# Kernel tuning notes

Measured on AMD Instinct MI355X. Metric: run time of the kernel, lower is better.

The kernel has to match this reference:

```python
import jax, jax.numpy as jnp
import numpy as np

H, DK = 8, 64  # n_head, d_k = n_feat // n_head
SCALE = 1.0 / np.sqrt(DK)


def setup_inputs() -> dict:
    key0 = jax.random.key(0)
    ks = jax.random.split(key0, 13)
    B, N, T1, T2, F = 16, 4, 256, 1024, 512
    query = jax.random.normal(ks[0], (B, T1, F), jnp.float32)
    key = jax.random.normal(ks[1], (B, N, T2, F), jnp.float32)
    value = jax.random.normal(ks[2], (B, N, T2, F), jnp.float32)
    mask_audio = jax.random.randint(ks[3], (B, N, 1, T2), 0, 2).astype(jnp.int32)
    # guarantee each candidate row has at least one valid key frame
    mask_audio = mask_audio.at[..., 0].set(1)
    mask_spk = jax.random.randint(ks[4], (B, N), 0, 2).astype(jnp.int32)
    # guarantee at least one valid candidate per batch item (avoids all -inf softmax)
    mask_spk = mask_spk.at[:, 0].set(1)
    s = 1.0 / np.sqrt(F)
    Wq = jax.random.normal(ks[5], (F, F), jnp.float32) * s
    bq = jax.random.normal(ks[6], (F,), jnp.float32) * 0.01
    Wk = jax.random.normal(ks[7], (F, F), jnp.float32) * s
    bk = jax.random.normal(ks[8], (F,), jnp.float32) * 0.01
    Wv = jax.random.normal(ks[9], (F, F), jnp.float32) * s
    bv = jax.random.normal(ks[10], (F,), jnp.float32) * 0.01
    Wo = jax.random.normal(ks[11], (F, F), jnp.float32) * s
    bo = jax.random.normal(ks[12], (F,), jnp.float32) * 0.01
    return dict(query=query, key=key, value=value, mask_audio=mask_audio,
                mask_spk=mask_spk, Wq=Wq, bq=bq, Wk=Wk, bk=bk, Wv=Wv, bv=bv,
                Wo=Wo, bo=bo)


def reference(query, key, value, mask_audio, mask_spk, Wq, bq, Wk, bk, Wv, bv, Wo, bo):
    B, T1, F = query.shape
    N, T2 = key.shape[1], key.shape[2]
    # projections (torch Linear: x @ W.T + b)
    q = (query @ Wq.T + bq).reshape(B, T1, H, DK)                 # (B,T1,H,DK)
    k = (key @ Wk.T + bk).reshape(B, N, T2, H, DK)                # (B,N,T2,H,DK)
    v = (value @ Wv.T + bv).reshape(B, N, T2, H, DK)
    # stage 1: intra-candidate temporal attention
    scores = jnp.einsum('bthd,bnshd->bnhts', q, k) * SCALE        # (B,N,H,T1,T2)
    ma = (mask_audio != 0)[:, :, None, :, :]                      # (B,N,1,1,T2)
    scores = jnp.where(ma, scores, -jnp.inf)
    attn1 = jnp.where(ma, jax.nn.softmax(scores, axis=-1), 0.0)
    phone = jnp.einsum('bnhts,bnshd->bnhtd', attn1, v)            # (B,N,H,T1,DK)
    # stage 2: inter-candidate attention
    ss = jnp.einsum('bthd,bnhtd->bthn', q, phone) * SCALE         # (B,T1,H,N)
    ms = (mask_spk != 0)[:, None, None, :]                        # (B,1,1,N)
    ss = jnp.where(ms, ss, -jnp.inf)
    attn2 = jnp.where(ms, jax.nn.softmax(ss, axis=-1), 0.0)
    x = jnp.einsum('bthn,bnhtd->bthd', attn2, phone).reshape(B, T1, H * DK)
    return x @ Wo.T + bo
```

## Files before the change

### kernel.cpp

```cpp
#include <hip/hip_runtime.h>
#include <hip/hip_bf16.h>
#include <math.h>

typedef __attribute__((ext_vector_type(4))) float  f32x4;
typedef __attribute__((ext_vector_type(4))) int    i32x4;
typedef __attribute__((ext_vector_type(8))) __bf16 bf16x8;
typedef __attribute__((ext_vector_type(8))) unsigned short u16x8;
typedef __attribute__((ext_vector_type(4))) unsigned short u16x4;

#define DEV static __device__ __forceinline__

#if __has_builtin(__builtin_amdgcn_permlane32_swap) && __has_builtin(__builtin_amdgcn_permlane16_swap)
#define HAVE_PERMLANE 1
#else
#define HAVE_PERMLANE 0
#endif

namespace {

constexpr int kB = 16, kT1 = 256, kF = 512, kN = 4, kT2 = 1024, kH = 8;
constexpr float kSCALE = 0.125f;
constexpr float kLOG2E = 1.4426950408889634f;

DEV unsigned short f2bf(float f) {
  union { __bf16 h; unsigned short u; } c; c.h = (__bf16)f; return c.u;
}
DEV float bf2f(unsigned short h) {
  union { unsigned u; float f; } c; c.u = ((unsigned)h) << 16;
  return c.f;
}

DEV void async_copy16(const void* g, void* l) {
  __builtin_amdgcn_global_load_lds(
      (const __attribute__((address_space(1))) unsigned int*)g,
      (__attribute__((address_space(3))) unsigned int*)l, 16, 0, 0);
}

DEV bf16x8 cvt8(f32x4 lo, f32x4 hi) {
  bf16x8 r;
  r[0] = (__bf16)lo[0]; r[1] = (__bf16)lo[1]; r[2] = (__bf16)lo[2]; r[3] = (__bf16)lo[3];
  r[4] = (__bf16)hi[0]; r[5] = (__bf16)hi[1]; r[6] = (__bf16)hi[2]; r[7] = (__bf16)hi[3];
  return r;
}

__global__ __launch_bounds__(256) void convert_w(
    const float* __restrict__ w0, const float* __restrict__ w1,
    const float* __restrict__ w2, const float* __restrict__ w3,
    unsigned short* __restrict__ o0, unsigned short* __restrict__ o1,
    unsigned short* __restrict__ o2, unsigned short* __restrict__ o3) {
  const int r = blockIdx.x >> 8;
  const int l = ((blockIdx.x & 255) * 256 + threadIdx.x) * 4;
  const float* src = r == 0 ? w0 : r == 1 ? w1 : r == 2 ? w2 : w3;
  unsigned short* dst = r == 0 ? o0 : r == 1 ? o1 : r == 2 ? o2 : o3;
  const float4 v = *(const float4*)(src + l);
  u16x4 q; q[0] = f2bf(v.x); q[1] = f2bf(v.y); q[2] = f2bf(v.z); q[3] = f2bf(v.w);
  *(u16x4*)(dst + l) = q;
}

template<int MODE>
__global__ __launch_bounds__(512, 2) void gemm256(
    const float* __restrict__ A, const unsigned short* __restrict__ Wb,
    const float* __restrict__ bias, unsigned short* __restrict__ outv) {
  __shared__ __align__(16) unsigned short As[2][256 * 64];
  __shared__ __align__(16) unsigned short Ws[2][256 * 64];
  const int t = threadIdx.x, lane = t & 63, wave = t >> 6;
  const int rb = blockIdx.x >> 1, cb = blockIdx.x & 1;
  const int wr = wave >> 2, wc = wave & 3;
  const int lq = lane & 15, lg = lane >> 4;
  const int arg = t >> 4, as16 = t & 15;

  f32x4 acc[8][4];
#pragma unroll
  for (int i = 0; i < 8; ++i)
#pragma unroll
    for (int j = 0; j < 4; ++j) acc[i][j] = f32x4{0.f, 0.f, 0.f, 0.f};

  f32x4 areg[8];
  bf16x8 af[4][2], bf[4][2];

#define A_ISSUE(kt)                                                             \
  do {                                                                          \
    _Pragma("unroll")                                                           \
    for (int j_ = 0; j_ < 8; ++j_)                                              \
      areg[j_] = *(const f32x4*)(A + (size_t)(rb * 256 + j_ * 32 + arg) * kF +  \
                                 (kt) * 64 + as16 * 4);                         \
  } while (0)

#define A_WRITE(dst)                                                            \
  do {                                                                          \
    _Pragma("unroll")                                                           \
    for (int j_ = 0; j_ < 8; ++j_) {                                            \
      const int row_ = j_ * 32 + arg;                                           \
      const int off_ = row_ * 64 + (((as16 >> 1) ^ (row_ & 7)) << 3) + (as16 & 1) * 4; \
      u16x4 pk_;                                                                \
      pk_[0] = f2bf(areg[j_][0]); pk_[1] = f2bf(areg[j_][1]);                   \
      pk_[2] = f2bf(areg[j_][2]); pk_[3] = f2bf(areg[j_][3]);                   \
      *(u16x4*)&(dst)[off_] = pk_;                                              \
    }                                                                           \
  } while (0)

#define W_ISSUE(kt, dst)                                                        \
  do {                                                                          \
    _Pragma("unroll")                                                           \
    for (int j_ = 0; j_ < 4; ++j_) {                                            \
      const int sidx_ = t + j_ * 512;                                           \
      const int row_ = sidx_ >> 3, s_ = sidx_ & 7;                              \
      async_copy16(Wb + (size_t)(cb * 256 + row_) * kF + (kt) * 64 +            \
                       ((s_ ^ (row_ & 7)) << 3),                                \
                   (dst) + (size_t)(j_ * 512 + wave * 64) * 8);                 \
    }                                                                           \
  } while (0)

#define RD_BF(pw)                                                               \
  do {                                                                          \
    _Pragma("unroll")                                                           \
    for (int n_ = 0; n_ < 4; ++n_) {                                            \
      const int br_ = wc * 64 + n_ * 16 + lq, x7_ = br_ & 7;                    \
      bf[n_][0] = *(const bf16x8*)&(pw)[br_ * 64 + ((lg ^ x7_) << 3)];          \
      bf[n_][1] = *(const bf16x8*)&(pw)[br_ * 64 + (((4 + lg) ^ x7_) << 3)];    \
    }                                                                           \
  } while (0)

#define RD_AF(pa, mb)                                                           \
  do {                                                                          \
    _Pragma("unroll")                                                           \
    for (int m_ = 0; m_ < 4; ++m_) {                                            \
      const int ar_ = wr * 128 + ((mb) + m_) * 16 + lq, x7_ = ar_ & 7;          \
      af[m_][0] = *(const bf16x8*)&(pa)[ar_ * 64 + ((lg ^ x7_) << 3)];          \
      af[m_][1] = *(const bf16x8*)&(pa)[ar_ * 64 + (((4 + lg) ^ x7_) << 3)];    \
    }                                                                           \
  } while (0)

#define MM(mb)                                                                  \
  do {                                                                          \
    _Pragma("unroll")                                                           \
    for (int kk_ = 0; kk_ < 2; ++kk_)                                           \
      _Pragma("unroll")                                                         \
      for (int m_ = 0; m_ < 4; ++m_)                                            \
        _Pragma("unroll")                                                       \
        for (int n_ = 0; n_ < 4; ++n_)                                          \
          acc[(mb) + m_][n_] = __builtin_amdgcn_mfma_f32_16x16x32_bf16(         \
              af[m_][kk_], bf[n_][kk_], acc[(mb) + m_][n_], 0, 0, 0);           \
  } while (0)

#define VMW(n) asm volatile("s_waitcnt vmcnt(" #n ")" ::: "memory")
#define LKW  asm volatile("s_waitcnt lgkmcnt(0)" ::: "memory")
#define SB   __builtin_amdgcn_sched_barrier(0)
#define BAR  do { __builtin_amdgcn_s_barrier(); __builtin_amdgcn_sched_barrier(0); } while (0)

  A_ISSUE(0); W_ISSUE(0, Ws[0]);
  VMW(4); SB;
  A_WRITE(As[0]);
  LKW;

  unsigned short *pa = As[0], *qa = As[1], *pw = Ws[0], *qw = Ws[1];
#pragma unroll 1
  for (int kt = 0; kt < 8; ++kt) {
    if (kt < 7) {
      A_ISSUE(kt + 1);
      W_ISSUE(kt + 1, qw);
      VMW(12); SB;
    } else {
      VMW(0); SB;
    }
    BAR;
    RD_BF(pw); RD_AF(pa, 0);
    LKW; SB;
    __builtin_amdgcn_s_setprio(1); MM(0); __builtin_amdgcn_s_setprio(0); SB;
    RD_AF(pa, 4);
    LKW; SB;
    __builtin_amdgcn_s_setprio(1); MM(4); __builtin_amdgcn_s_setprio(0); SB;
    if (kt < 7) {
      VMW(4); SB;
      A_WRITE(qa);
    }
    LKW; BAR;
    { unsigned short* x = pa; pa = qa; qa = x; }
    { unsigned short* x = pw; pw = qw; qw = x; }
  }

#undef A_ISSUE
#undef A_WRITE
#undef W_ISSUE
#undef RD_BF
#undef RD_AF
#undef MM
#undef VMW
#undef LKW
#undef SB
#undef BAR

  float bs4[4];
#pragma unroll
  for (int n = 0; n < 4; ++n) bs4[n] = bias[cb * 256 + wc * 64 + n * 16 + lq];

#pragma unroll
  for (int m = 0; m < 8; ++m) {
    const int row0 = rb * 256 + wr * 128 + m * 16 + lg * 4;
    const int bn = row0 >> 10, t2 = row0 & 1023;
#pragma unroll
    for (int n = 0; n < 4; ++n) {
      const int col = cb * 256 + wc * 64 + n * 16 + lq;
      const int h = col >> 6, d = col & 63;
      if (MODE == 3) {
        u16x4 pv;
#pragma unroll
        for (int j = 0; j < 4; ++j) pv[j] = f2bf(acc[m][n][j] + bs4[n]);
        *(u16x4*)&outv[(((size_t)(bn * kH + h)) * 64 + d) * kT2 + t2] = pv;
      } else {
#pragma unroll
        for (int j = 0; j < 4; ++j)
          outv[(((size_t)(bn * kH + h)) * kT2 + t2 + j) * 64 + d] =
              f2bf(acc[m][n][j] + bs4[n]);
      }
    }
  }
}

template<int MODE>
__global__ __launch_bounds__(256, 2) void gemm_mixed(
    const float* __restrict__ A, const unsigned short* __restrict__ Wb,
    const float* __restrict__ bias, void* __restrict__ outv, int nrb) {
  __shared__ __align__(16) unsigned short As[2][128 * 64];
  __shared__ __align__(16) unsigned short Bs[3][128 * 64];
  const int t = threadIdx.x, lane = t & 63, wave = t >> 6;
  const int w = blockIdx.x;
  const int xcd = w & 7, s = w >> 3;
  const int rb = xcd * (nrb >> 3) + (s >> 2);
  const int cb = s & 3;
  const int wr = wave >> 1, wc = wave & 1;
  const int lq = lane & 15, lg = lane >> 4;

  const int arow = t >> 1, ah = (t & 1) * 4;
  const float* aptr = A + (size_t)(rb * 128 + arow) * kF + ah * 8;

  f32x4 acc[4][4];
#pragma unroll
  for (int i = 0; i < 4; ++i)
#pragma unroll
    for (int j = 0; j < 4; ++j) acc[i][j] = f32x4{0.f, 0.f, 0.f, 0.f};

  f32x4 arA[8], arB[8];
  bf16x8 af[4][2], bfr[4][2];

#define A_LOAD(kb, ar)                                                          \
  do {                                                                          \
    const f32x4* p_ = (const f32x4*)(aptr + (kb) * 64);                         \
    ar[0]=p_[0]; ar[1]=p_[1]; ar[2]=p_[2]; ar[3]=p_[3];                         \
    ar[4]=p_[4]; ar[5]=p_[5]; ar[6]=p_[6]; ar[7]=p_[7];                         \
  } while (0)

#define A_CVT(ar, dst)                                                          \
  do {                                                                          \
    _Pragma("unroll")                                                           \
    for (int j_ = 0; j_ < 4; ++j_)                                              \
      *(bf16x8*)&(dst)[arow * 64 + (((ah + j_) ^ (arow & 7)) << 3)] =           \
          cvt8(ar[2*j_], ar[2*j_+1]);                                           \
  } while (0)

#define W_STAGE2(kb, dst)                                                       \
  do {                                                                          \
    _Pragma("unroll")                                                           \
    for (int i_ = 0; i_ < 4; ++i_) {                                            \
      const int sidx_ = t + i_ * 256;                                           \
      const int row_ = sidx_ >> 3;                                              \
      const int gseg_ = (sidx_ & 7) ^ (row_ & 7);                               \
      async_copy16(Wb + (size_t)(cb * 128 + row_) * kF + (kb) * 64 + gseg_ * 8, \
                   (dst) + (size_t)(i_ * 256 + wave * 64) * 8);                 \
    }                                                                           \
  } while (0)

#define FRAG(Ap, Wp)                                                            \
  do {                                                                          \
    _Pragma("unroll")                                                           \
    for (int m_ = 0; m_ < 4; ++m_) {                                            \
      const int ar_ = wr * 64 + m_ * 16 + lq, x7_ = ar_ & 7;                    \
      af[m_][0] = *(const bf16x8*)&(Ap)[ar_ * 64 + ((lg       ^ x7_) << 3)];    \
      af[m_][1] = *(const bf16x8*)&(Ap)[ar_ * 64 + (((lg + 4) ^ x7_) << 3)];    \
    }                                                                           \
    _Pragma("unroll")                                                           \
    for (int n_ = 0; n_ < 4; ++n_) {                                            \
      const int br_ = wc * 64 + n_ * 16 + lq, x7_ = br_ & 7;                    \
      bfr[n_][0] = *(const bf16x8*)&(Wp)[br_ * 64 + ((lg       ^ x7_) << 3)];   \
      bfr[n_][1] = *(const bf16x8*)&(Wp)[br_ * 64 + (((lg + 4) ^ x7_) << 3)];   \
    }                                                                           \
  } while (0)

#define MFMA8                                                                   \
  do {                                                                          \
    _Pragma("unroll")                                                           \
    for (int kk_ = 0; kk_ < 2; ++kk_)                                           \
      _Pragma("unroll")                                                         \
      for (int m_ = 0; m_ < 4; ++m_)                                            \
        _Pragma("unroll")                                                       \
        for (int n_ = 0; n_ < 4; ++n_)                                          \
          acc[m_][n_] = __builtin_amdgcn_mfma_f32_16x16x32_bf16(                \
              af[m_][kk_], bfr[n_][kk_], acc[m_][n_], 0, 0, 0);                 \
  } while (0)

#define VMW(n) asm volatile("s_waitcnt vmcnt(" #n ")" ::: "memory")
#define LKW    asm volatile("s_waitcnt lgkmcnt(0)" ::: "memory")
#define BAR    do { __builtin_amdgcn_s_barrier(); __builtin_amdgcn_sched_barrier(0); } while (0)

  A_LOAD(0, arA); A_LOAD(1, arB);
  W_STAGE2(0, Bs[0]); W_STAGE2(1, Bs[1]);
  VMW(16);
  A_CVT(arA, As[0]);
  LKW; BAR;
  A_LOAD(2, arA); W_STAGE2(2, Bs[2]);
  FRAG(As[0], Bs[0]); MFMA8;
  VMW(12); A_CVT(arB, As[1]); LKW; BAR;
  A_LOAD(3, arB); W_STAGE2(3, Bs[0]);
  FRAG(As[1], Bs[1]); MFMA8;
  VMW(12); A_CVT(arA, As[0]); LKW; BAR;
  A_LOAD(4, arA); W_STAGE2(4, Bs[1]);
  FRAG(As[0], Bs[2]); MFMA8;
  VMW(12); A_CVT(arB, As[1]); LKW; BAR;
  A_LOAD(5, arB); W_STAGE2(5, Bs[2]);
  FRAG(As[1], Bs[0]); MFMA8;
  VMW(12); A_CVT(arA, As[0]); LKW; BAR;
  A_LOAD(6, arA); W_STAGE2(6, Bs[0]);
  FRAG(As[0], Bs[1]); MFMA8;
  VMW(12); A_CVT(arB, As[1]); LKW; BAR;
  A_LOAD(7, arB); W_STAGE2(7, Bs[1]);
  FRAG(As[1], Bs[2]); MFMA8;
  VMW(12); A_CVT(arA, As[0]); LKW; BAR;
  FRAG(As[0], Bs[0]); MFMA8;
  VMW(0); A_CVT(arB, As[1]); LKW; BAR;
  FRAG(As[1], Bs[1]); MFMA8;

#undef A_LOAD
#undef A_CVT
#undef W_STAGE2
#undef FRAG
#undef MFMA8
#undef VMW
#undef LKW
#undef BAR

  float bs[4];
#pragma unroll
  for (int n2 = 0; n2 < 4; ++n2) bs[n2] = bias[cb*128 + wc*64 + n2*16 + lq];

#pragma unroll
  for (int m = 0; m < 4; ++m) {
#pragma unroll
    for (int n2 = 0; n2 < 4; ++n2) {
      const int col = cb*128 + wc*64 + n2*16 + lq;
      const int row0 = rb*128 + wr*64 + m*16 + lg*4;
#pragma unroll
      for (int j = 0; j < 4; ++j) {
        const int row = row0 + j;
        const float v = acc[m][n2][j] + bs[n2];
        if (MODE == 2) {
          ((float*)outv)[(size_t)row * kF + col] = v;
        } else {
          const int h = col >> 6, d = col & 63;
          const int b = row >> 8, t1i = row & 255;
          ((unsigned short*)outv)[(((size_t)(b * kH + h)) * kT1 + t1i) * 64 + d] = f2bf(v);
        }
      }
    }
  }
}

__global__ __launch_bounds__(512, 4) void attn_kernel(
    const unsigned short* __restrict__ qh, const unsigned short* __restrict__ kh,
    const unsigned short* __restrict__ vt, const int* __restrict__ mask_audio,
    unsigned short* __restrict__ phone) {
  __shared__ __align__(16) unsigned short Ks[3][64 * 64];
  __shared__ __align__(16) unsigned short Vs[3][64 * 64];
  __shared__ float Mbias[1024];
  const int t = threadIdx.x;
  const int lane = t & 63, wave = t >> 6;
  const int lq = lane & 15, lg = lane >> 4;
  const int bid = blockIdx.x;
  const int h = bid & 7, n = (bid >> 3) & 3, b = bid >> 5;
  const size_t qbase  = ((size_t)(b * kH + h)) * kT1 * 64;
  const size_t kvbase = ((size_t)((b * kN + n) * kH + h)) * kT2 * 64;
  const int* mbase = mask_audio + (size_t)(b * kN + n) * kT2;

  const int srow = (wave << 3) + (lane >> 3);
  const int sgx = ((lane & 7) ^ (srow & 7)) << 3;

#define STAGE_KV(c, kd, vd)                                                       \
  do {                                                                            \
    async_copy16(kh + kvbase + ((size_t)(((c) << 6) + srow) << 6) + sgx,          \
                 (kd) + (wave << 9));                                             \
    async_copy16(vt + kvbase + ((size_t)srow << 10) + ((c) << 6) + sgx,           \
                 (vd) + (wave << 9));                                             \
  } while (0)

  {
    const int i0 = t * 2;
    const int m0 = mbase[i0], m1 = mbase[i0 + 1];
    Mbias[i0]     = m0 ? 0.f : -1e30f;
    Mbias[i0 + 1] = m1 ? 0.f : -1e30f;
  }

  bf16x8 qf[2][2];
#pragma unroll
  for (int qt = 0; qt < 2; ++qt) {
    const unsigned short* qp = qh + qbase + ((size_t)((wave << 5) + (qt << 4) + lq) << 6);
    qf[qt][0] = *(const bf16x8*)(qp + (lg << 3));
    qf[qt][1] = *(const bf16x8*)(qp + 32 + (lg << 3));
  }

  unsigned short *kb0 = Ks[0], *kb1 = Ks[1], *kb2 = Ks[2];
  unsigned short *vb0 = Vs[0], *vb1 = Vs[1], *vb2 = Vs[2];

  STAGE_KV(0, kb0, vb0);
  STAGE_KV(1, kb1, vb1);
  asm volatile("s_waitcnt lgkmcnt(0)" ::: "memory");

  f32x4 of[2][4];
  float l1[2];
#pragma unroll
  for (int qt = 0; qt < 2; ++qt) {
    l1[qt] = 0.f;
#pragma unroll
    for (int fd = 0; fd < 4; ++fd) of[qt][fd] = f32x4{0.f, 0.f, 0.f, 0.f};
  }
  const float sc2 = kSCALE * kLOG2E;

#pragma unroll 1
  for (int c = 0; c < 16; ++c) {
    if (c < 15) asm volatile("s_waitcnt vmcnt(2)" ::: "memory");
    else        asm volatile("s_waitcnt vmcnt(0)" ::: "memory");
    __builtin_amdgcn_s_barrier();
    __builtin_amdgcn_sched_barrier(0);

    const float* mrow = Mbias + (c << 6);

    bf16x8 kf[4][2];
#pragma unroll
    for (int kt = 0; kt < 4; ++kt) {
      const int kr = kt * 16 + lq, x7 = kr & 7;
      kf[kt][0] = *(const bf16x8*)&kb0[kr * 64 + ((lg       ^ x7) << 3)];
      kf[kt][1] = *(const bf16x8*)&kb0[kr * 64 + (((lg + 4) ^ x7) << 3)];
    }

#pragma unroll
    for (int qt = 0; qt < 2; ++qt) {
      f32x4 sT[4];
#pragma unroll
      for (int kt = 0; kt < 4; ++kt) {
        f32x4 sv = f32x4{0.f, 0.f, 0.f, 0.f};
        sv = __builtin_amdgcn_mfma_f32_16x16x32_bf16(kf[kt][0], qf[qt][0], sv, 0, 0, 0);
        sv = __builtin_amdgcn_mfma_f32_16x16x32_bf16(kf[kt][1], qf[qt][1], sv, 0, 0, 0);
        sT[kt] = sv;
      }
      float pf[16];
#pragma unroll
      for (int kt = 0; kt < 4; ++kt) {
        const f32x4 mk = *(const f32x4*)&mrow[kt * 16 + lg * 4];
#pragma unroll
        for (int j = 0; j < 4; ++j)
          pf[kt*4+j] = exp2f(fmaf(sT[kt][j], sc2, mk[j]));
      }
      const float a0 = (pf[0] + pf[1]) + (pf[2] + pf[3]);
      const float a1 = (pf[4] + pf[5]) + (pf[6] + pf[7]);
      const float a2 = (pf[8] + pf[9]) + (pf[10] + pf[11]);
      const float a3 = (pf[12] + pf[13]) + (pf[14] + pf[15]);
      l1[qt] += (a0 + a1) + (a2 + a3);
      unsigned pk[8];
#pragma unroll
      for (int kt = 0; kt < 4; ++kt) {
        pk[2*kt]   = (unsigned)f2bf(pf[4*kt+0]) | ((unsigned)f2bf(pf[4*kt+1]) << 16);
        pk[2*kt+1] = (unsigned)f2bf(pf[4*kt+2]) | ((unsigned)f2bf(pf[4*kt+3]) << 16);
      }
      unsigned am0[4], am1[4];
#if HAVE_PERMLANE
      {
        auto x0p = __builtin_amdgcn_permlane32_swap((int)pk[0], (int)pk[2], false, false);
        auto y0p = __builtin_amdgcn_permlane16_swap(x0p[0], x0p[1], false, false);
        am0[0] = (unsigned)y0p[0]; am0[2] = (unsigned)y0p[1];
        auto x1p = __builtin_amdgcn_permlane32_swap((int)pk[1], (int)pk[3], false, false);
        auto y1p = __builtin_amdgcn_permlane16_swap(x1p[0], x1p[1], false, false);
        am0[1] = (unsigned)y1p[0]; am0[3] = (unsigned)y1p[1];
        auto x2p = __builtin_amdgcn_permlane32_swap((int)pk[4], (int)pk[6], false, false);
        auto y2p = __builtin_amdgcn_permlane16_swap(x2p[0], x2p[1], false, false);
        am1[0] = (unsigned)y2p[0]; am1[2] = (unsigned)y2p[1];
        auto x3p = __builtin_amdgcn_permlane32_swap((int)pk[5], (int)pk[7], false, false);
        auto y3p = __builtin_amdgcn_permlane16_swap(x3p[0], x3p[1], false, false);
        am1[1] = (unsigned)y3p[0]; am1[3] = (unsigned)y3p[1];
      }
#else
      {
        const int srcbase = (2 * (lg & 1)) * 16 + lq;
#pragma unroll
        for (int u = 0; u < 4; ++u) {
          const int src = srcbase + (u >> 1) * 16;
          const unsigned va0 = __shfl(pk[(u & 1)],     src);
          const unsigned vb0s = __shfl(pk[2 + (u & 1)], src);
          am0[u] = (lg & 2) ? vb0s : va0;
          const unsigned va1 = __shfl(pk[4 + (u & 1)], src);
          const unsigned vb1s = __shfl(pk[6 + (u & 1)], src);
          am1[u] = (lg & 2) ? vb1s : va1;
        }
      }
#endif
      union { unsigned u[4]; bf16x8 v; } A0, A1;
#pragma unroll
      for (int u = 0; u < 4; ++u) { A0.u[u] = am0[u]; A1.u[u] = am1[u]; }
#pragma unroll
      for (int fd = 0; fd < 4; ++fd) {
        const int d = fd * 16 + lq, x7d = d & 7;
        const bf16x8 vB0 = *(const bf16x8*)&vb0[d * 64 + ((lg       ^ x7d) << 3)];
        const bf16x8 vB1 = *(const bf16x8*)&vb0[d * 64 + (((lg + 4) ^ x7d) << 3)];
        of[qt][fd] = __builtin_amdgcn_mfma_f32_16x16x32_bf16(A0.v, vB0, of[qt][fd], 0, 0, 0);
        of[qt][fd] = __builtin_amdgcn_mfma_f32_16x16x32_bf16(A1.v, vB1, of[qt][fd], 0, 0, 0);
      }
    }

    if (c < 14) STAGE_KV(c + 2, kb2, vb2);
    { unsigned short* x = kb0; kb0 = kb1; kb1 = kb2; kb2 = x; }
    { unsigned short* x = vb0; vb0 = vb1; vb1 = vb2; vb2 = x; }
  }
#undef STAGE_KV

#pragma unroll
  for (int qt = 0; qt < 2; ++qt) {
    l1[qt] += __shfl_xor(l1[qt], 16);
    l1[qt] += __shfl_xor(l1[qt], 32);
  }
  const size_t phbase = ((size_t)((b * kN + n) * kH + h)) * kT1 * 64;
#pragma unroll
  for (int qt = 0; qt < 2; ++qt) {
    const float li0 = 1.f / __shfl(l1[qt], lg*4 + 0);
    const float li1 = 1.f / __shfl(l1[qt], lg*4 + 1);
    const float li2 = 1.f / __shfl(l1[qt], lg*4 + 2);
    const float li3 = 1.f / __shfl(l1[qt], lg*4 + 3);
#pragma unroll
    for (int fd = 0; fd < 4; ++fd) {
      const int d = fd * 16 + lq;
      const size_t rowb = phbase + (size_t)((wave << 5) + qt*16 + lg*4) * 64 + d;
      phone[rowb]       = f2bf(of[qt][fd][0] * li0);
      phone[rowb + 64]  = f2bf(of[qt][fd][1] * li1);
      phone[rowb + 128] = f2bf(of[qt][fd][2] * li2);
      phone[rowb + 192] = f2bf(of[qt][fd][3] * li3);
    }
  }
}

__global__ __launch_bounds__(256) void stage2_kernel(
    const unsigned short* __restrict__ qh, const unsigned short* __restrict__ phone,
    const int* __restrict__ mask_spk, float* __restrict__ x) {
  const int t = threadIdx.x, lane = t & 63, wave = t >> 6;
  const int wid = blockIdx.x * 4 + wave;
  const int h = wid & 7;
  const int bt = wid >> 3;
  const int t1i = bt & 255, b = bt >> 8;
  const int d = lane;
  const float q = bf2f(qh[(((size_t)(b * kH + h)) * kT1 + t1i) * 64 + d]);
  float ph[4], ss[4];
#pragma unroll
  for (int n = 0; n < 4; ++n) {
    ph[n] = bf2f(phone[(((size_t)((b * kN + n) * kH + h)) * kT1 + t1i) * 64 + d]);
    float sv = q * ph[n];
#pragma unroll
    for (int o = 1; o < 64; o <<= 1) sv += __shfl_xor(sv, o);
    ss[n] = sv * kSCALE;
  }
  int msk[4];
#pragma unroll
  for (int n = 0; n < 4; ++n) msk[n] = mask_spk[b * kN + n];
  float mx = -INFINITY;
#pragma unroll
  for (int n = 0; n < 4; ++n) if (msk[n]) mx = fmaxf(mx, ss[n]);
  float e[4], sum = 0.f;
#pragma unroll
  for (int n = 0; n < 4; ++n) { const float v = msk[n] ? __expf(ss[n] - mx) : 0.f; e[n] = v; sum += v; }
  float xo = 0.f;
#pragma unroll
  for (int n = 0; n < 4; ++n) xo += e[n] * ph[n];
  xo /= sum;
  x[((size_t)(b * kT1 + t1i)) * kF + h * 64 + d] = xo;
}

}

extern "C" void kernel_launch(void* const* d_in, const int* in_sizes, int n_in,
                              void* d_out, int out_size, void* d_ws, size_t ws_size,
                              hipStream_t stream) {
  (void)in_sizes; (void)n_in; (void)out_size; (void)ws_size;
  const float* query = (const float*)d_in[0];
  const float* key   = (const float*)d_in[1];
  const float* value = (const float*)d_in[2];
  const int* mask_audio = (const int*)d_in[3];
  const int* mask_spk   = (const int*)d_in[4];
  const float* Wq = (const float*)d_in[5];  const float* bq = (const float*)d_in[6];
  const float* Wk = (const float*)d_in[7];  const float* bk = (const float*)d_in[8];
  const float* Wv = (const float*)d_in[9];  const float* bv = (const float*)d_in[10];
  const float* Wo = (const float*)d_in[11]; const float* bo = (const float*)d_in[12];
  float* out = (float*)d_out;

  unsigned short* qws  = (unsigned short*)d_ws;
  unsigned short* kws  = qws  + (size_t)kB * kH * kT1 * 64;
  unsigned short* vws  = kws  + (size_t)kB * kN * kH * kT2 * 64;
  unsigned short* phws = vws  + (size_t)kB * kN * kH * kT2 * 64;
  float*          xws  = (float*)(phws + (size_t)kB * kN * kH * kT1 * 64);
  unsigned short* wqb  = (unsigned short*)(xws + (size_t)kB * kT1 * kF);
  unsigned short* wkb  = wqb + (size_t)kF * kF;
  unsigned short* wvb  = wkb + (size_t)kF * kF;
  unsigned short* wob  = wvb + (size_t)kF * kF;

  convert_w<<<1024, 256, 0, stream>>>(Wq, Wk, Wv, Wo, wqb, wkb, wvb, wob);
  gemm_mixed<0><<<kB * kT1 / 128 * 4, 256, 0, stream>>>(query, wqb, bq, qws, kB * kT1 / 128);
  gemm256<1><<<kB * kN * kT2 / 256 * 2, 512, 0, stream>>>(key,   wkb, bk, kws);
  gemm256<3><<<kB * kN * kT2 / 256 * 2, 512, 0, stream>>>(value, wvb, bv, vws);
  attn_kernel<<<kB * kN * kH, 512, 0, stream>>>(qws, kws, vws, mask_audio, phws);
  stage2_kernel<<<kB * kT1 * kH / 4, 256, 0, stream>>>(qws, phws, mask_spk, xws);
  gemm_mixed<2><<<kB * kT1 / 128 * 4, 256, 0, stream>>>(xws, wob, bo, out, kB * kT1 / 128);
}
```

Measured before the change: 279.5 us.

## Split attention query rows across two blocks with XCD-aware block swizzle

The attention kernel now launches twice as many blocks, each handling 128 query rows (16 per wave) instead of 256, so every wave processes one query tile per K/V chunk instead of two. A block-index swizzle is meant to map the two halves of the same (b,n,h) onto the same XCD so the K/V re-reads can hit in L2. The goal is more blocks in flight on the GPU and lower per-wave register pressure. The cost is that K/V tiles are staged from global memory twice, and each wave does less MFMA work per barrier.

```diff
diff --git a/kernel.cpp b/kernel.cpp
--- a/kernel.cpp
+++ b/kernel.cpp
@@ -374,8 +374,10 @@
   const int t = threadIdx.x;
   const int lane = t & 63, wave = t >> 6;
   const int lq = lane & 15, lg = lane >> 4;
-  const int bid = blockIdx.x;
-  const int h = bid & 7, n = (bid >> 3) & 3, b = bid >> 5;
+  const int w = blockIdx.x;
+  const int swz = (w & 7) * 128 + (w >> 3);
+  const int qb = swz & 1, bnh = swz >> 1;
+  const int h = bnh & 7, n = (bnh >> 3) & 3, b = bnh >> 5;
   const size_t qbase  = ((size_t)(b * kH + h)) * kT1 * 64;
   const size_t kvbase = ((size_t)((b * kN + n) * kH + h)) * kT2 * 64;
   const int* mbase = mask_audio + (size_t)(b * kN + n) * kT2;
@@ -398,12 +400,12 @@
     Mbias[i0 + 1] = m1 ? 0.f : -1e30f;
   }
 
-  bf16x8 qf[2][2];
-#pragma unroll
-  for (int qt = 0; qt < 2; ++qt) {
-    const unsigned short* qp = qh + qbase + ((size_t)((wave << 5) + (qt << 4) + lq) << 6);
-    qf[qt][0] = *(const bf16x8*)(qp + (lg << 3));
-    qf[qt][1] = *(const bf16x8*)(qp + 32 + (lg << 3));
+  bf16x8 qf0, qf1;
+  {
+    const unsigned short* qp = qh + qbase +
+        ((size_t)((qb << 7) + (wave << 4) + lq) << 6);
+    qf0 = *(const bf16x8*)(qp + (lg << 3));
+    qf1 = *(const bf16x8*)(qp + 32 + (lg << 3));
   }
 
   unsigned short *kb0 = Ks[0], *kb1 = Ks[1], *kb2 = Ks[2];
@@ -413,14 +415,10 @@
   STAGE_KV(1, kb1, vb1);
   asm volatile("s_waitcnt lgkmcnt(0)" ::: "memory");
 
-  f32x4 of[2][4];
-  float l1[2];
-#pragma unroll
-  for (int qt = 0; qt < 2; ++qt) {
-    l1[qt] = 0.f;
-#pragma unroll
-    for (int fd = 0; fd < 4; ++fd) of[qt][fd] = f32x4{0.f, 0.f, 0.f, 0.f};
-  }
+  f32x4 of[4];
+  float l1 = 0.f;
+#pragma unroll
+  for (int fd = 0; fd < 4; ++fd) of[fd] = f32x4{0.f, 0.f, 0.f, 0.f};
   const float sc2 = kSCALE * kLOG2E;
 
 #pragma unroll 1
@@ -432,85 +430,77 @@
 
     const float* mrow = Mbias + (c << 6);
 
-    bf16x8 kf[4][2];
+    f32x4 sT[4];
 #pragma unroll
     for (int kt = 0; kt < 4; ++kt) {
       const int kr = kt * 16 + lq, x7 = kr & 7;
-      kf[kt][0] = *(const bf16x8*)&kb0[kr * 64 + ((lg       ^ x7) << 3)];
-      kf[kt][1] = *(const bf16x8*)&kb0[kr * 64 + (((lg + 4) ^ x7) << 3)];
-    }
-
-#pragma unroll
-    for (int qt = 0; qt < 2; ++qt) {
-      f32x4 sT[4];
-#pragma unroll
-      for (int kt = 0; kt < 4; ++kt) {
-        f32x4 sv = f32x4{0.f, 0.f, 0.f, 0.f};
-        sv = __builtin_amdgcn_mfma_f32_16x16x32_bf16(kf[kt][0], qf[qt][0], sv, 0, 0, 0);
-        sv = __builtin_amdgcn_mfma_f32_16x16x32_bf16(kf[kt][1], qf[qt][1], sv, 0, 0, 0);
-        sT[kt] = sv;
+      const bf16x8 kf0 = *(const bf16x8*)&kb0[kr * 64 + ((lg       ^ x7) << 3)];
+      const bf16x8 kf1 = *(const bf16x8*)&kb0[kr * 64 + (((lg + 4) ^ x7) << 3)];
+      f32x4 sv = f32x4{0.f, 0.f, 0.f, 0.f};
+      sv = __builtin_amdgcn_mfma_f32_16x16x32_bf16(kf0, qf0, sv, 0, 0, 0);
+      sv = __builtin_amdgcn_mfma_f32_16x16x32_bf16(kf1, qf1, sv, 0, 0, 0);
+      sT[kt] = sv;
+    }
+    float pf[16];
+#pragma unroll
+    for (int kt = 0; kt < 4; ++kt) {
+      const f32x4 mk = *(const f32x4*)&mrow[kt * 16 + lg * 4];
+#pragma unroll
+      for (int j = 0; j < 4; ++j)
+        pf[kt*4+j] = exp2f(fmaf(sT[kt][j], sc2, mk[j]));
+    }
+    const float a0 = (pf[0] + pf[1]) + (pf[2] + pf[3]);
+    const float a1 = (pf[4] + pf[5]) + (pf[6] + pf[7]);
+    const float a2 = (pf[8] + pf[9]) + (pf[10] + pf[11]);
+    const float a3 = (pf[12] + pf[13]) + (pf[14] + pf[15]);
+    l1 += (a0 + a1) + (a2 + a3);
+    unsigned pk[8];
+#pragma unroll
+    for (int kt = 0; kt < 4; ++kt) {
+      pk[2*kt]   = (unsigned)f2bf(pf[4*kt+0]) | ((unsigned)f2bf(pf[4*kt+1]) << 16);
+      pk[2*kt+1] = (unsigned)f2bf(pf[4*kt+2]) | ((unsigned)f2bf(pf[4*kt+3]) << 16);
+    }
+    unsigned am0[4], am1[4];
+#if HAVE_PERMLANE
+    {
+      auto x0p = __builtin_amdgcn_permlane32_swap((int)pk[0], (int)pk[2], false, false);
+      auto y0p = __builtin_amdgcn_permlane16_swap(x0p[0], x0p[1], false, false);
+      am0[0] = (unsigned)y0p[0]; am0[2] = (unsigned)y0p[1];
+      auto x1p = __builtin_amdgcn_permlane32_swap((int)pk[1], (int)pk[3], false, false);
+      auto y1p = __builtin_amdgcn_permlane16_swap(x1p[0], x1p[1], false, false);
+      am0[1] = (unsigned)y1p[0]; am0[3] = (unsigned)y1p[1];
+      auto x2p = __builtin_amdgcn_permlane32_swap((int)pk[4], (int)pk[6], false, false);
+      auto y2p = __builtin_amdgcn_permlane16_swap(x2p[0], x2p[1], false, false);
+      am1[0] = (unsigned)y2p[0]; am1[2] = (unsigned)y2p[1];
+      auto x3p = __builtin_amdgcn_permlane32_swap((int)pk[5], (int)pk[7], false, false);
+      auto y3p = __builtin_amdgcn_permlane16_swap(x3p[0], x3p[1], false, false);
+      am1[1] = (unsigned)y3p[0]; am1[3] = (unsigned)y3p[1];
+    }
+#else
+    {
+      const int srcbase = (2 * (lg & 1)) * 16 + lq;
+#pragma unroll
+      for (int u = 0; u < 4; ++u) {
+        const int src = srcbase + (u >> 1) * 16;
+        const unsigned va0 = __shfl(pk[(u & 1)],     src);
+        const unsigned vb0s = __shfl(pk[2 + (u & 1)], src);
+        am0[u] = (lg & 2) ? vb0s : va0;
+        const unsigned va1 = __shfl(pk[4 + (u & 1)], src);
+        const unsigned vb1s = __shfl(pk[6 + (u & 1)], src);
+        am1[u] = (lg & 2) ? vb1s : va1;
       }
-      float pf[16];
-#pragma unroll
-      for (int kt = 0; kt < 4; ++kt) {
-        const f32x4 mk = *(const f32x4*)&mrow[kt * 16 + lg * 4];
-#pragma unroll
-        for (int j = 0; j < 4; ++j)
-          pf[kt*4+j] = exp2f(fmaf(sT[kt][j], sc2, mk[j]));
-      }
-      const float a0 = (pf[0] + pf[1]) + (pf[2] + pf[3]);
-      const float a1 = (pf[4] + pf[5]) + (pf[6] + pf[7]);
-      const float a2 = (pf[8] + pf[9]) + (pf[10] + pf[11]);
-      const float a3 = (pf[12] + pf[13]) + (pf[14] + pf[15]);
-      l1[qt] += (a0 + a1) + (a2 + a3);
-      unsigned pk[8];
-#pragma unroll
-      for (int kt = 0; kt < 4; ++kt) {
-        pk[2*kt]   = (unsigned)f2bf(pf[4*kt+0]) | ((unsigned)f2bf(pf[4*kt+1]) << 16);
-        pk[2*kt+1] = (unsigned)f2bf(pf[4*kt+2]) | ((unsigned)f2bf(pf[4*kt+3]) << 16);
-      }
-      unsigned am0[4], am1[4];
-#if HAVE_PERMLANE
-      {
-        auto x0p = __builtin_amdgcn_permlane32_swap((int)pk[0], (int)pk[2], false, false);
-        auto y0p = __builtin_amdgcn_permlane16_swap(x0p[0], x0p[1], false, false);
-        am0[0] = (unsigned)y0p[0]; am0[2] = (unsigned)y0p[1];
-        auto x1p = __builtin_amdgcn_permlane32_swap((int)pk[1], (int)pk[3], false, false);
-        auto y1p = __builtin_amdgcn_permlane16_swap(x1p[0], x1p[1], false, false);
-        am0[1] = (unsigned)y1p[0]; am0[3] = (unsigned)y1p[1];
-        auto x2p = __builtin_amdgcn_permlane32_swap((int)pk[4], (int)pk[6], false, false);
-        auto y2p = __builtin_amdgcn_permlane16_swap(x2p[0], x2p[1], false, false);
-        am1[0] = (unsigned)y2p[0]; am1[2] = (unsigned)y2p[1];
-        auto x3p = __builtin_amdgcn_permlane32_swap((int)pk[5], (int)pk[7], false, false);
-        auto y3p = __builtin_amdgcn_permlane16_swap(x3p[0], x3p[1], false, false);
-        am1[1] = (unsigned)y3p[0]; am1[3] = (unsigned)y3p[1];
-      }
-#else
-      {
-        const int srcbase = (2 * (lg & 1)) * 16 + lq;
-#pragma unroll
-        for (int u = 0; u < 4; ++u) {
-          const int src = srcbase + (u >> 1) * 16;
-          const unsigned va0 = __shfl(pk[(u & 1)],     src);
-          const unsigned vb0s = __shfl(pk[2 + (u & 1)], src);
-          am0[u] = (lg & 2) ? vb0s : va0;
-          const unsigned va1 = __shfl(pk[4 + (u & 1)], src);
-          const unsigned vb1s = __shfl(pk[6 + (u & 1)], src);
-          am1[u] = (lg & 2) ? vb1s : va1;
-        }
-      }
+    }
 #endif
-      union { unsigned u[4]; bf16x8 v; } A0, A1;
-#pragma unroll
-      for (int u = 0; u < 4; ++u) { A0.u[u] = am0[u]; A1.u[u] = am1[u]; }
-#pragma unroll
-      for (int fd = 0; fd < 4; ++fd) {
-        const int d = fd * 16 + lq, x7d = d & 7;
-        const bf16x8 vB0 = *(const bf16x8*)&vb0[d * 64 + ((lg       ^ x7d) << 3)];
-        const bf16x8 vB1 = *(const bf16x8*)&vb0[d * 64 + (((lg + 4) ^ x7d) << 3)];
-        of[qt][fd] = __builtin_amdgcn_mfma_f32_16x16x32_bf16(A0.v, vB0, of[qt][fd], 0, 0, 0);
-        of[qt][fd] = __builtin_amdgcn_mfma_f32_16x16x32_bf16(A1.v, vB1, of[qt][fd], 0, 0, 0);
-      }
+    union { unsigned u[4]; bf16x8 v; } A0, A1;
+#pragma unroll
+    for (int u = 0; u < 4; ++u) { A0.u[u] = am0[u]; A1.u[u] = am1[u]; }
+#pragma unroll
+    for (int fd = 0; fd < 4; ++fd) {
+      const int d = fd * 16 + lq, x7d = d & 7;
+      const bf16x8 vB0 = *(const bf16x8*)&vb0[d * 64 + ((lg       ^ x7d) << 3)];
+      const bf16x8 vB1 = *(const bf16x8*)&vb0[d * 64 + (((lg + 4) ^ x7d) << 3)];
+      of[fd] = __builtin_amdgcn_mfma_f32_16x16x32_bf16(A0.v, vB0, of[fd], 0, 0, 0);
+      of[fd] = __builtin_amdgcn_mfma_f32_16x16x32_bf16(A1.v, vB1, of[fd], 0, 0, 0);
     }
 
     if (c < 14) STAGE_KV(c + 2, kb2, vb2);
@@ -519,27 +509,22 @@
   }
 #undef STAGE_KV
 
-#pragma unroll
-  for (int qt = 0; qt < 2; ++qt) {
-    l1[qt] += __shfl_xor(l1[qt], 16);
-    l1[qt] += __shfl_xor(l1[qt], 32);
-  }
+  l1 += __shfl_xor(l1, 16);
+  l1 += __shfl_xor(l1, 32);
   const size_t phbase = ((size_t)((b * kN + n) * kH + h)) * kT1 * 64;
-#pragma unroll
-  for (int qt = 0; qt < 2; ++qt) {
-    const float li0 = 1.f / __shfl(l1[qt], lg*4 + 0);
-    const float li1 = 1.f / __shfl(l1[qt], lg*4 + 1);
-    const float li2 = 1.f / __shfl(l1[qt], lg*4 + 2);
-    const float li3 = 1.f / __shfl(l1[qt], lg*4 + 3);
-#pragma unroll
-    for (int fd = 0; fd < 4; ++fd) {
-      const int d = fd * 16 + lq;
-      const size_t rowb = phbase + (size_t)((wave << 5) + qt*16 + lg*4) * 64 + d;
-      phone[rowb]       = f2bf(of[qt][fd][0] * li0);
-      phone[rowb + 64]  = f2bf(of[qt][fd][1] * li1);
-      phone[rowb + 128] = f2bf(of[qt][fd][2] * li2);
-      phone[rowb + 192] = f2bf(of[qt][fd][3] * li3);
-    }
+  const float li0 = 1.f / __shfl(l1, lg*4 + 0);
+  const float li1 = 1.f / __shfl(l1, lg*4 + 1);
+  const float li2 = 1.f / __shfl(l1, lg*4 + 2);
+  const float li3 = 1.f / __shfl(l1, lg*4 + 3);
+#pragma unroll
+  for (int fd = 0; fd < 4; ++fd) {
+    const int d = fd * 16 + lq;
+    const size_t rowb = phbase +
+        (size_t)((qb << 7) + (wave << 4) + lg*4) * 64 + d;
+    phone[rowb]       = f2bf(of[fd][0] * li0);
+    phone[rowb + 64]  = f2bf(of[fd][1] * li1);
+    phone[rowb + 128] = f2bf(of[fd][2] * li2);
+    phone[rowb + 192] = f2bf(of[fd][3] * li3);
   }
 }
 
@@ -609,7 +594,7 @@
   gemm_mixed<0><<<kB * kT1 / 128 * 4, 256, 0, stream>>>(query, wqb, bq, qws, kB * kT1 / 128);
   gemm256<1><<<kB * kN * kT2 / 256 * 2, 512, 0, stream>>>(key,   wkb, bk, kws);
   gemm256<3><<<kB * kN * kT2 / 256 * 2, 512, 0, stream>>>(value, wvb, bv, vws);
-  attn_kernel<<<kB * kN * kH, 512, 0, stream>>>(qws, kws, vws, mask_audio, phws);
+  attn_kernel<<<kB * kN * kH * 2, 512, 0, stream>>>(qws, kws, vws, mask_audio, phws);
   stage2_kernel<<<kB * kT1 * kH / 4, 256, 0, stream>>>(qws, phws, mask_spk, xws);
   gemm_mixed<2><<<kB * kT1 / 128 * 4, 256, 0, stream>>>(xws, wob, bo, out, kB * kT1 / 128);
 }
```

Result: faster. 261.4 us (median of 2 runs) (-6.5%).
